# Optimization experiments

Hardware: AMD Instinct MI355X
Metric: run time of the kernel (lower is better)

## Reference

```python
import jax, jax.numpy as jnp
import numpy as np

N, H, W = 128, 128, 128
K = 9          # 3x3 kernel points
DIL = 3        # dilation of the deformable conv


def conv2d(x, w, pad, dil):
    # x: [N,C,H,W], w: [O,I,kh,kw]
    return jax.lax.conv_general_dilated(
        x, w, (1, 1), [(pad, pad), (pad, pad)], rhs_dilation=(dil, dil),
        dimension_numbers=("NCHW", "OIHW", "NCHW"))


def _bilinear_one(img, py, px):
    # img: [C,H,W]; py, px: [K,H,W] sample coords. Zero outside borders (DCNv2 semantics).
    Hh, Ww = img.shape[1], img.shape[2]
    y0f = jnp.floor(py)
    x0f = jnp.floor(px)
    y0 = y0f.astype(jnp.int32)
    x0 = x0f.astype(jnp.int32)
    ly = (py - y0f)[None]   # [1,K,H,W]
    lx = (px - x0f)[None]

    def gather(yi, xi):
        valid = ((yi >= 0) & (yi < Hh) & (xi >= 0) & (xi < Ww)).astype(img.dtype)
        yc = jnp.clip(yi, 0, Hh - 1)
        xc = jnp.clip(xi, 0, Ww - 1)
        return img[:, yc, xc] * valid[None]   # [C,K,H,W]

    v00 = gather(y0, x0)
    v01 = gather(y0, x0 + 1)
    v10 = gather(y0 + 1, x0)
    v11 = gather(y0 + 1, x0 + 1)
    return (v00 * (1 - ly) * (1 - lx) + v01 * (1 - ly) * lx
            + v10 * ly * (1 - lx) + v11 * ly * lx)


def modulated_deform_conv(x, offset, mod, w, b):
    # x: [N,C,H,W]; offset: [N,2K,H,W] with (dy,dx) interleaved per kernel point
    # (standard DCNv2 channel layout); mod: [N,K,H,W]; w: [O,C,3,3]; b: [O]
    Np, C, Hh, Ww = x.shape
    dy = offset[:, 0::2]   # [N,K,H,W]
    dx = offset[:, 1::2]
    base_y = ((jnp.repeat(jnp.arange(3), 3) - 1) * DIL).astype(x.dtype)  # [K]
    base_x = ((jnp.tile(jnp.arange(3), 3) - 1) * DIL).astype(x.dtype)
    gy = jnp.arange(Hh, dtype=x.dtype).reshape(1, 1, Hh, 1)
    gx = jnp.arange(Ww, dtype=x.dtype).reshape(1, 1, 1, Ww)
    py = dy + base_y.reshape(1, K, 1, 1) + gy   # [N,K,H,W]
    px = dx + base_x.reshape(1, K, 1, 1) + gx
    samp = jax.vmap(_bilinear_one)(x, py, px)   # [N,C,K,H,W]
    samp = samp * mod[:, None]                  # sigmoid modulation
    out = jnp.einsum("nckij,ock->noij", samp, w.reshape(w.shape[0], C, K))
    return out + b.reshape(1, -1, 1, 1)


def setup_inputs() -> dict:
    key = jax.random.key(0)
    ks = jax.random.split(key, 12)
    f32 = jnp.float32
    return {
        "mask": jax.random.normal(ks[0], (N, 1, H, W), f32),
        "x": jax.random.normal(ks[1], (N, 8, H, W), f32),
        "w1": jax.random.normal(ks[2], (2, 9, 3, 3), f32) * 0.1,      # conv1x1_1 (3x3)
        "b1": jnp.zeros((2,), f32),
        "w_off": jax.random.normal(ks[3], (27, 2, 3, 3), f32) * 0.05,  # offset/mask conv
        "w_dcn": jax.random.normal(ks[4], (2, 2, 3, 3), f32) * 0.2,    # deform conv weight
        "b_dcn": jnp.zeros((2,), f32),
        "w2": jax.random.normal(ks[5], (2, 2, 1, 1), f32) * 0.5,       # conv1x1_2
        "b2": jnp.zeros((2,), f32),
        "fc1_w": jax.random.normal(ks[6], (2048, 2 * 64 * 64), f32) * 0.01,
        "fc1_b": jnp.zeros((2048,), f32),
        "fc2_w": jax.random.normal(ks[7], (1024, 2048), f32) * 0.02,
        "fc2_b": jnp.zeros((1024,), f32),
        "io_w": jax.random.normal(ks[8], (1, 1024), f32) * 0.01,
        "io_b": jnp.zeros((1,), f32),
    }


def reference(mask, x, w1, b1, w_off, w_dcn, b_dcn, w2, b2,
              fc1_w, fc1_b, fc2_w, fc2_b, io_w, io_b):
    z = jnp.concatenate([x, mask], axis=1)                    # [N,9,H,W]
    h = conv2d(z, w1, 1, 1) + b1.reshape(1, -1, 1, 1)          # [N,2,H,W]
    om = conv2d(h, w_off, 3, 3)                               # [N,27,H,W], bias=False
    ox, oy, mm = jnp.split(om, 3, axis=1)
    offset = jnp.concatenate([ox, oy], axis=1)                # [N,18,H,W]
    mm = jax.nn.sigmoid(mm)                                   # [N,9,H,W]
    h = modulated_deform_conv(h, offset, mm, w_dcn, b_dcn)    # [N,2,H,W]
    h = jax.nn.relu(conv2d(h, w2, 0, 1) + b2.reshape(1, -1, 1, 1))
    Np, C, Hh, Ww = h.shape                                   # adaptive max pool to 64x64
    h = h.reshape(Np, C, 64, Hh // 64, 64, Ww // 64).max(axis=(3, 5))
    h = h.reshape(Np, -1)                                     # [N, 8192]
    h = jax.nn.relu(h @ fc1_w.T + fc1_b)
    h = jax.nn.relu(h @ fc2_w.T + fc2_b)
    return jax.nn.sigmoid(h @ io_w.T + io_b)                  # [N,1]
```

## Files before the change

### kernel.cpp

```cpp
#include <hip/hip_runtime.h>
#include <math.h>

#define NB   128
#define HH   128
#define WW   128
#define HW   (HH*WW)
#define POOLD 64
#define FC1_IN  8192
#define FC1_OUT 2048
#define FC2_OUT 1024

#define H1_OFF    0
#define POOL_OFF  4194304
#define FC1_OFF   5242880
#define FC2_OFF   5505024

__global__ __launch_bounds__(256) void conv1_kernel(
    const float* __restrict__ xin, const float* __restrict__ mask,
    const float* __restrict__ w1, const float* __restrict__ b1,
    float* __restrict__ h1)
{
    __shared__ float sw[164];
    __shared__ float sh[9][10][132];

    int tid = threadIdx.x;
    int n   = blockIdx.y;
    int r0  = blockIdx.x * 8;

    if (tid < 162) sw[tid] = w1[tid];
    if (tid < 2)   sw[162 + tid] = b1[tid];

    for (int i = tid; i < 90; i += 256) {
        int c  = i / 10;
        int ry = i - c * 10;
        sh[c][ry][0]   = 0.f;
        sh[c][ry][129] = 0.f;
    }

    for (int idx = tid; idx < 2880; idx += 256) {
        int c   = idx / 320;
        int rem = idx - c * 320;
        int ry  = rem >> 5;
        int x4  = (rem & 31) << 2;
        int g   = r0 - 1 + ry;
        float4 v = make_float4(0.f, 0.f, 0.f, 0.f);
        if (g >= 0 && g < HH) {
            const float* src = (c < 8) ? (xin + ((size_t)n * 8 + c) * HW)
                                       : (mask + (size_t)n * HW);
            v = *(const float4*)(src + (size_t)g * WW + x4);
        }
        float* d = &sh[c][ry][x4 + 1];
        d[0] = v.x; d[1] = v.y; d[2] = v.z; d[3] = v.w;
    }
    __syncthreads();

    int x  = tid & 127;
    int yb = (tid >> 7) * 4;

    float acc[4][2];
    #pragma unroll
    for (int r = 0; r < 4; ++r) { acc[r][0] = sw[162]; acc[r][1] = sw[163]; }

    for (int c = 0; c < 9; ++c) {
        float v[6][3];
        #pragma unroll
        for (int iy = 0; iy < 6; ++iy)
            #pragma unroll
            for (int kx = 0; kx < 3; ++kx)
                v[iy][kx] = sh[c][yb + iy][x + kx];
        #pragma unroll
        for (int r = 0; r < 4; ++r)
            #pragma unroll
            for (int ky = 0; ky < 3; ++ky)
                #pragma unroll
                for (int kx = 0; kx < 3; ++kx) {
                    float t = v[r + ky][kx];
                    acc[r][0] += t * sw[c * 9 + ky * 3 + kx];
                    acc[r][1] += t * sw[81 + c * 9 + ky * 3 + kx];
                }
    }

    #pragma unroll
    for (int r = 0; r < 4; ++r) {
        size_t base = (size_t)n * (2 * HW) + (size_t)(r0 + yb + r) * WW + x;
        h1[base]      = acc[r][0];
        h1[base + HW] = acc[r][1];
    }
}

#define HALO 8

__device__ __forceinline__ void fetch2(
    const float* __restrict__ sh, const float* __restrict__ h0,
    const float* __restrict__ hb, int row_lo, int row_hi,
    int yi, int xi, float& a, float& b)
{
    a = 0.f; b = 0.f;
    if (yi < 0 || yi >= HH || xi < 0 || xi >= WW) return;
    if (yi >= row_lo && yi < row_hi) {
        const float* p = sh + ((size_t)(yi - row_lo) * WW + xi) * 2;
        a = p[0]; b = p[1];
    } else {
        a = h0[yi * WW + xi];
        b = hb[yi * WW + xi];
    }
}

__global__ __launch_bounds__(256, 4) void fused_dcn_kernel(
    const float* __restrict__ h1,
    const float* __restrict__ w_off,
    const float* __restrict__ w_dcn,
    const float* __restrict__ b_dcn,
    const float* __restrict__ w2,
    const float* __restrict__ b2,
    float* __restrict__ pooled)
{
    __shared__ float sh[32 * WW * 2];
    __shared__ float sw[530];

    int tid = threadIdx.x;
    int n   = blockIdx.y;
    int r0  = blockIdx.x * 16;

    for (int i = tid; i < 530; i += 256) {
        float v;
        if (i < 486)      v = w_off[i];
        else if (i < 522) v = w_dcn[i - 486];
        else if (i < 526) v = w2[i - 522];
        else if (i < 528) v = b_dcn[i - 526];
        else              v = b2[i - 528];
        sw[i] = v;
    }

    int row_lo = r0 - HALO;       if (row_lo < 0)   row_lo = 0;
    int row_hi = r0 + 16 + HALO;  if (row_hi > HH)  row_hi = HH;
    int rows = row_hi - row_lo;

    const float* h0 = h1 + (size_t)n * (2 * HW);
    const float* hb = h0 + HW;

    for (int idx = tid; idx < rows * 32; idx += 256) {
        int ry = idx >> 5;
        int x4 = (idx & 31) << 2;
        const float4 a = *(const float4*)(h0 + (size_t)(row_lo + ry) * WW + x4);
        const float4 b = *(const float4*)(hb + (size_t)(row_lo + ry) * WW + x4);
        float* d = sh + ((size_t)ry * WW + x4) * 2;
        d[0] = a.x; d[1] = b.x; d[2] = a.y; d[3] = b.y;
        d[4] = a.z; d[5] = b.z; d[6] = a.w; d[7] = b.w;
    }
    __syncthreads();

    const float* WOFF = sw;
    const float* WDCN = sw + 486;
    const float* W2   = sw + 522;
    const float* BDCN = sw + 526;
    const float* B2   = sw + 528;

    int pc  = tid & 63;
    int prb = blockIdx.x * 8 + (tid >> 6);

    #pragma unroll 1
    for (int i = 0; i < 2; ++i) {
        int pr = prb + 4 * i;
        float m0 = -1e30f, m1 = -1e30f;

        #pragma unroll 1
        for (int s = 0; s < 4; ++s) {
            int y = pr * 2 + (s >> 1);
            int x = pc * 2 + (s & 1);

            float hvx[9], hvy[9];
            #pragma unroll
            for (int t = 0; t < 9; ++t) {
                int yy = y + (t / 3 - 1) * 3;
                int xx = x + (t % 3 - 1) * 3;
                float a = 0.f, b = 0.f;
                if (yy >= 0 && yy < HH && xx >= 0 && xx < WW) {
                    const float* p = sh + ((size_t)(yy - row_lo) * WW + xx) * 2;
                    a = p[0]; b = p[1];
                }
                hvx[t] = a; hvy[t] = b;
            }

            float acc0 = 0.f, acc1 = 0.f;
            #pragma unroll 1
            for (int k = 0; k < 9; ++k) {
                const float* wy = WOFF + (2 * k) * 18;
                const float* wx = WOFF + (2 * k + 1) * 18;
                const float* wm = WOFF + (18 + k) * 18;
                float dyv = 0.f, dxv = 0.f, mv = 0.f;
                #pragma unroll
                for (int t = 0; t < 9; ++t) {
                    float ha = hvx[t], hcb = hvy[t];
                    dyv += ha * wy[t] + hcb * wy[9 + t];
                    dxv += ha * wx[t] + hcb * wx[9 + t];
                    mv  += ha * wm[t] + hcb * wm[9 + t];
                }
                float mod = 1.f / (1.f + __expf(-mv));

                float py  = (float)(y + (k / 3 - 1) * 3) + dyv;
                float pxx = (float)(x + (k % 3 - 1) * 3) + dxv;
                float y0f = floorf(py), x0f = floorf(pxx);
                int   y0 = (int)y0f,   x0 = (int)x0f;
                float ly = py - y0f,   lx = pxx - x0f;

                float a00, b00, a01, b01, a10, b10, a11, b11;
                fetch2(sh, h0, hb, row_lo, row_hi, y0,     x0,     a00, b00);
                fetch2(sh, h0, hb, row_lo, row_hi, y0,     x0 + 1, a01, b01);
                fetch2(sh, h0, hb, row_lo, row_hi, y0 + 1, x0,     a10, b10);
                fetch2(sh, h0, hb, row_lo, row_hi, y0 + 1, x0 + 1, a11, b11);

                float w00 = (1.f - ly) * (1.f - lx);
                float w01 = (1.f - ly) * lx;
                float w10 = ly * (1.f - lx);
                float w11 = ly * lx;
                float sA = (w00 * a00 + w01 * a01 + w10 * a10 + w11 * a11) * mod;
                float sB = (w00 * b00 + w01 * b01 + w10 * b10 + w11 * b11) * mod;

                acc0 += WDCN[k]      * sA + WDCN[9 + k]  * sB;
                acc1 += WDCN[18 + k] * sA + WDCN[27 + k] * sB;
            }

            float v0 = acc0 + BDCN[0];
            float v1 = acc1 + BDCN[1];
            float u0 = fmaxf(W2[0] * v0 + W2[1] * v1 + B2[0], 0.f);
            float u1 = fmaxf(W2[2] * v0 + W2[3] * v1 + B2[1], 0.f);
            m0 = fmaxf(m0, u0);
            m1 = fmaxf(m1, u1);
        }

        size_t pb = (size_t)n * FC1_IN + (size_t)pr * POOLD + pc;
        pooled[pb]        = m0;
        pooled[pb + 4096] = m1;
    }
}

__global__ void init_bias2_kernel(
    float* __restrict__ o1, const float* __restrict__ bb1,
    float* __restrict__ o2, const float* __restrict__ bb2)
{
    int i = blockIdx.x * blockDim.x + threadIdx.x;
    if (i < NB * FC1_OUT) o1[i] = bb1[i & (FC1_OUT - 1)];
    if (i < NB * FC2_OUT) o2[i] = bb2[i & (FC2_OUT - 1)];
}

typedef __bf16 bf16x8 __attribute__((ext_vector_type(8)));
typedef float  f32x4  __attribute__((ext_vector_type(4)));

#define LDT 40

__device__ __forceinline__ unsigned short f2bf(float f) {
    unsigned int u = __float_as_uint(f);
    return (unsigned short)((u + 0x7fffu + ((u >> 16) & 1u)) >> 16);
}

__global__ __launch_bounds__(256) void gemm_bf16_splitk(
    const float* __restrict__ A, const float* __restrict__ B,
    float* __restrict__ C, int K, int Nc, int kchunk, int relu_a)
{
    __shared__ __align__(16) unsigned short As[128 * LDT];
    __shared__ __align__(16) unsigned short Bs[64 * LDT];

    int tid = threadIdx.x;
    int jt  = blockIdx.x;
    int k0  = blockIdx.y * kchunk;
    int iters = kchunk >> 5;

    int t8  = tid >> 3;
    int c16 = (tid & 7) << 2;

    const float* Ag = A + (size_t)t8 * K + k0 + c16;
    const float* Bg = B + (size_t)(jt * 64 + t8) * K + k0 + c16;

    float4 pa[4]; float4 pb[2];
    #pragma unroll
    for (int p = 0; p < 4; ++p) pa[p] = *(const float4*)(Ag + (size_t)(p * 32) * K);
    #pragma unroll
    for (int p = 0; p < 2; ++p) pb[p] = *(const float4*)(Bg + (size_t)(p * 32) * K);

    int lane = tid & 63;
    int w    = tid >> 6;
    int quad = lane >> 4;
    int r    = lane & 15;

    f32x4 acc[2][4];
    #pragma unroll
    for (int mt = 0; mt < 2; ++mt)
        #pragma unroll
        for (int nt = 0; nt < 4; ++nt)
            acc[mt][nt] = (f32x4){0.f, 0.f, 0.f, 0.f};

    for (int it = 0; it < iters; ++it) {
        #pragma unroll
        for (int p = 0; p < 4; ++p) {
            float4 v = pa[p];
            if (relu_a) {
                v.x = fmaxf(v.x, 0.f); v.y = fmaxf(v.y, 0.f);
                v.z = fmaxf(v.z, 0.f); v.w = fmaxf(v.w, 0.f);
            }
            ushort4 s = make_ushort4(f2bf(v.x), f2bf(v.y), f2bf(v.z), f2bf(v.w));
            *(ushort4*)&As[(t8 + p * 32) * LDT + c16] = s;
        }
        #pragma unroll
        for (int p = 0; p < 2; ++p) {
            float4 v = pb[p];
            ushort4 s = make_ushort4(f2bf(v.x), f2bf(v.y), f2bf(v.z), f2bf(v.w));
            *(ushort4*)&Bs[(t8 + p * 32) * LDT + c16] = s;
        }
        __syncthreads();

        if (it + 1 < iters) {
            Ag += 32; Bg += 32;
            #pragma unroll
            for (int p = 0; p < 4; ++p) pa[p] = *(const float4*)(Ag + (size_t)(p * 32) * K);
            #pragma unroll
            for (int p = 0; p < 2; ++p) pb[p] = *(const float4*)(Bg + (size_t)(p * 32) * K);
        }

        bf16x8 af[2];
        #pragma unroll
        for (int mt = 0; mt < 2; ++mt)
            af[mt] = *(const bf16x8*)&As[(w * 32 + mt * 16 + r) * LDT + quad * 8];
        bf16x8 bfr[4];
        #pragma unroll
        for (int nt = 0; nt < 4; ++nt)
            bfr[nt] = *(const bf16x8*)&Bs[(nt * 16 + r) * LDT + quad * 8];

        #pragma unroll
        for (int mt = 0; mt < 2; ++mt)
            #pragma unroll
            for (int nt = 0; nt < 4; ++nt)
                acc[mt][nt] = __builtin_amdgcn_mfma_f32_16x16x32_bf16(
                    af[mt], bfr[nt], acc[mt][nt], 0, 0, 0);

        __syncthreads();
    }

    #pragma unroll
    for (int mt = 0; mt < 2; ++mt) {
        int mrow = w * 32 + mt * 16 + quad * 4;
        #pragma unroll
        for (int nt = 0; nt < 4; ++nt) {
            int col = jt * 64 + nt * 16 + r;
            #pragma unroll
            for (int i = 0; i < 4; ++i)
                atomicAdd(C + (size_t)(mrow + i) * Nc + col, acc[mt][nt][i]);
        }
    }
}

__global__ __launch_bounds__(256) void io_kernel(
    const float* __restrict__ fc2o, const float* __restrict__ io_w,
    const float* __restrict__ io_b, float* __restrict__ out)
{
    int n = blockIdx.x;
    int tid = threadIdx.x;
    float s = 0.f;
    #pragma unroll
    for (int k = tid; k < FC2_OUT; k += 256)
        s += fmaxf(fc2o[(size_t)n * FC2_OUT + k], 0.f) * io_w[k];
    #pragma unroll
    for (int off = 32; off > 0; off >>= 1)
        s += __shfl_down(s, off, 64);
    __shared__ float red[4];
    if ((tid & 63) == 0) red[tid >> 6] = s;
    __syncthreads();
    if (tid == 0) {
        float t = red[0] + red[1] + red[2] + red[3] + io_b[0];
        out[n] = 1.f / (1.f + expf(-t));
    }
}

extern "C" void kernel_launch(void* const* d_in, const int* in_sizes, int n_in,
                              void* d_out, int out_size, void* d_ws, size_t ws_size,
                              hipStream_t stream)
{
    const float* mask  = (const float*)d_in[0];
    const float* x     = (const float*)d_in[1];
    const float* w1    = (const float*)d_in[2];
    const float* b1    = (const float*)d_in[3];
    const float* w_off = (const float*)d_in[4];
    const float* w_dcn = (const float*)d_in[5];
    const float* b_dcn = (const float*)d_in[6];
    const float* w2    = (const float*)d_in[7];
    const float* b2    = (const float*)d_in[8];
    const float* fc1_w = (const float*)d_in[9];
    const float* fc1_b = (const float*)d_in[10];
    const float* fc2_w = (const float*)d_in[11];
    const float* fc2_b = (const float*)d_in[12];
    const float* io_w  = (const float*)d_in[13];
    const float* io_b  = (const float*)d_in[14];

    float* ws      = (float*)d_ws;
    float* h1      = ws + H1_OFF;
    float* pooled  = ws + POOL_OFF;
    float* fc1_out = ws + FC1_OFF;
    float* fc2_out = ws + FC2_OFF;
    float* out     = (float*)d_out;

    conv1_kernel<<<dim3(16, NB), 256, 0, stream>>>(x, mask, w1, b1, h1);

    fused_dcn_kernel<<<dim3(8, NB), 256, 0, stream>>>(
        h1, w_off, w_dcn, b_dcn, w2, b2, pooled);

    init_bias2_kernel<<<(NB * FC1_OUT + 255) / 256, 256, 0, stream>>>(
        fc1_out, fc1_b, fc2_out, fc2_b);

    gemm_bf16_splitk<<<dim3(FC1_OUT / 64, 16), 256, 0, stream>>>(
        pooled, fc1_w, fc1_out, FC1_IN, FC1_OUT, FC1_IN / 16, 0);

    gemm_bf16_splitk<<<dim3(FC2_OUT / 64, 16), 256, 0, stream>>>(
        fc1_out, fc2_w, fc2_out, FC1_OUT, FC2_OUT, FC1_OUT / 16, 1);

    io_kernel<<<NB, 256, 0, stream>>>(fc2_out, io_w, io_b, out);
}
```

Before: 334.2 us.

## Restructure DCN kernel to share offset weights across four pooled pixels

The loop order inside the fused DCN kernel is swapped so each kernel point k handles all four pixels of a 2x2 pool window together, which reuses each offset-conv weight load four times. Weights are repacked in shared memory as interleaved float2/float4. The shared tile gets zero padding columns and rows so the hot path can do unconditional float2 loads and a single bounds check per bilinear sample. The cost is higher register pressure, reflected in dropping launch_bounds occupancy from 4 to 3, plus a larger shared tile.

```diff
diff --git a/kernel.cpp b/kernel.cpp
--- a/kernel.cpp
+++ b/kernel.cpp
@@ -88,25 +88,15 @@
     }
 }
 
-#define HALO 8
-
-__device__ __forceinline__ void fetch2(
-    const float* __restrict__ sh, const float* __restrict__ h0,
-    const float* __restrict__ hb, int row_lo, int row_hi,
-    int yi, int xi, float& a, float& b)
-{
-    a = 0.f; b = 0.f;
-    if (yi < 0 || yi >= HH || xi < 0 || xi >= WW) return;
-    if (yi >= row_lo && yi < row_hi) {
-        const float* p = sh + ((size_t)(yi - row_lo) * WW + xi) * 2;
-        a = p[0]; b = p[1];
-    } else {
-        a = h0[yi * WW + xi];
-        b = hb[yi * WW + xi];
-    }
-}
-
-__global__ __launch_bounds__(256, 4) void fused_dcn_kernel(
+#define ROWB 32
+#define COLB 136
+
+__device__ __forceinline__ float gatg(const float* __restrict__ hc, int yi, int xi)
+{
+    return (yi >= 0 && yi < HH && xi >= 0 && xi < WW) ? hc[yi * WW + xi] : 0.f;
+}
+
+__global__ __launch_bounds__(256, 3) void fused_dcn_kernel(
     const float* __restrict__ h1,
     const float* __restrict__ w_off,
     const float* __restrict__ w_dcn,
@@ -115,46 +105,61 @@
     const float* __restrict__ b2,
     float* __restrict__ pooled)
 {
-    __shared__ float sh[32 * WW * 2];
-    __shared__ float sw[530];
+    __shared__ float sh[ROWB * COLB * 2];
+    __shared__ float swr[532];
 
     int tid = threadIdx.x;
     int n   = blockIdx.y;
     int r0  = blockIdx.x * 16;
-
-    for (int i = tid; i < 530; i += 256) {
-        float v;
-        if (i < 486)      v = w_off[i];
-        else if (i < 522) v = w_dcn[i - 486];
-        else if (i < 526) v = w2[i - 522];
-        else if (i < 528) v = b_dcn[i - 526];
-        else              v = b2[i - 528];
-        sw[i] = v;
-    }
-
-    int row_lo = r0 - HALO;       if (row_lo < 0)   row_lo = 0;
-    int row_hi = r0 + 16 + HALO;  if (row_hi > HH)  row_hi = HH;
-    int rows = row_hi - row_lo;
+    int row_base = r0 - 8;
+
+    for (int i = tid; i < 532; i += 256) {
+        float v = 0.f;
+        if (i < 486) {
+            int k = i / 54, r = i - k * 54;
+            int o = r / 18, q = r - o * 18;
+            int t = q >> 1, c = q & 1;
+            int srow = (o == 0) ? 2 * k : (o == 1) ? (2 * k + 1) : (18 + k);
+            v = w_off[srow * 18 + c * 9 + t];
+        } else if (i >= 488 && i < 524) {
+            int j = i - 488;
+            int k = j >> 2, oc = (j >> 1) & 1, c = j & 1;
+            v = w_dcn[oc * 18 + c * 9 + k];
+        } else if (i >= 524 && i < 528) v = w2[i - 524];
+        else if (i >= 528 && i < 530)   v = b_dcn[i - 528];
+        else if (i >= 530)              v = b2[i - 530];
+        swr[i] = v;
+    }
 
     const float* h0 = h1 + (size_t)n * (2 * HW);
     const float* hb = h0 + HW;
 
-    for (int idx = tid; idx < rows * 32; idx += 256) {
+    for (int idx = tid; idx < 1024; idx += 256) {
         int ry = idx >> 5;
         int x4 = (idx & 31) << 2;
-        const float4 a = *(const float4*)(h0 + (size_t)(row_lo + ry) * WW + x4);
-        const float4 b = *(const float4*)(hb + (size_t)(row_lo + ry) * WW + x4);
-        float* d = sh + ((size_t)ry * WW + x4) * 2;
+        int gy = row_base + ry;
+        float4 a = make_float4(0.f, 0.f, 0.f, 0.f);
+        float4 b = make_float4(0.f, 0.f, 0.f, 0.f);
+        if (gy >= 0 && gy < HH) {
+            a = *(const float4*)(h0 + (size_t)gy * WW + x4);
+            b = *(const float4*)(hb + (size_t)gy * WW + x4);
+        }
+        float* d = sh + ((size_t)ry * COLB + x4 + 4) * 2;
         d[0] = a.x; d[1] = b.x; d[2] = a.y; d[3] = b.y;
         d[4] = a.z; d[5] = b.z; d[6] = a.w; d[7] = b.w;
     }
+    {
+        int ry   = tid >> 3;
+        int pcix = tid & 7;
+        int rx   = (pcix < 4) ? pcix : (128 + pcix);
+        float* d = sh + ((size_t)ry * COLB + rx) * 2;
+        d[0] = 0.f; d[1] = 0.f;
+    }
     __syncthreads();
 
-    const float* WOFF = sw;
-    const float* WDCN = sw + 486;
-    const float* W2   = sw + 522;
-    const float* BDCN = sw + 526;
-    const float* B2   = sw + 528;
+    const float* W2   = swr + 524;
+    const float* BDCN = swr + 528;
+    const float* B2   = swr + 530;
 
     int pc  = tid & 63;
     int prb = blockIdx.x * 8 + (tid >> 6);
@@ -162,53 +167,73 @@
     #pragma unroll 1
     for (int i = 0; i < 2; ++i) {
         int pr = prb + 4 * i;
-        float m0 = -1e30f, m1 = -1e30f;
+
+        float2 hv[4][9];
+        #pragma unroll
+        for (int sp = 0; sp < 4; ++sp) {
+            int y  = pr * 2 + (sp >> 1);
+            int x  = pc * 2 + (sp & 1);
+            const float* base = sh + (((size_t)(y - row_base - 3)) * COLB + (x + 1)) * 2;
+            #pragma unroll
+            for (int ty = 0; ty < 3; ++ty)
+                #pragma unroll
+                for (int tx = 0; tx < 3; ++tx)
+                    hv[sp][ty * 3 + tx] =
+                        *(const float2*)(base + ((size_t)ty * 3 * COLB + tx * 3) * 2);
+        }
+
+        float acc0[4] = {0.f, 0.f, 0.f, 0.f};
+        float acc1[4] = {0.f, 0.f, 0.f, 0.f};
 
         #pragma unroll 1
-        for (int s = 0; s < 4; ++s) {
-            int y = pr * 2 + (s >> 1);
-            int x = pc * 2 + (s & 1);
-
-            float hvx[9], hvy[9];
+        for (int k = 0; k < 9; ++k) {
+            const float* wb = swr + k * 54;
+            float dyv[4] = {0.f, 0.f, 0.f, 0.f};
+            float dxv[4] = {0.f, 0.f, 0.f, 0.f};
+            float mv[4]  = {0.f, 0.f, 0.f, 0.f};
             #pragma unroll
             for (int t = 0; t < 9; ++t) {
-                int yy = y + (t / 3 - 1) * 3;
-                int xx = x + (t % 3 - 1) * 3;
-                float a = 0.f, b = 0.f;
-                if (yy >= 0 && yy < HH && xx >= 0 && xx < WW) {
-                    const float* p = sh + ((size_t)(yy - row_lo) * WW + xx) * 2;
-                    a = p[0]; b = p[1];
+                float2 wy = *(const float2*)(wb + t * 2);
+                float2 wx = *(const float2*)(wb + 18 + t * 2);
+                float2 wm = *(const float2*)(wb + 36 + t * 2);
+                #pragma unroll
+                for (int sp = 0; sp < 4; ++sp) {
+                    float2 h = hv[sp][t];
+                    dyv[sp] += h.x * wy.x + h.y * wy.y;
+                    dxv[sp] += h.x * wx.x + h.y * wx.y;
+                    mv[sp]  += h.x * wm.x + h.y * wm.y;
                 }
-                hvx[t] = a; hvy[t] = b;
             }
 
-            float acc0 = 0.f, acc1 = 0.f;
-            #pragma unroll 1
-            for (int k = 0; k < 9; ++k) {
-                const float* wy = WOFF + (2 * k) * 18;
-                const float* wx = WOFF + (2 * k + 1) * 18;
-                const float* wm = WOFF + (18 + k) * 18;
-                float dyv = 0.f, dxv = 0.f, mv = 0.f;
-                #pragma unroll
-                for (int t = 0; t < 9; ++t) {
-                    float ha = hvx[t], hcb = hvy[t];
-                    dyv += ha * wy[t] + hcb * wy[9 + t];
-                    dxv += ha * wx[t] + hcb * wx[9 + t];
-                    mv  += ha * wm[t] + hcb * wm[9 + t];
+            float4 wd = *(const float4*)(swr + 488 + k * 4);
+            int kdy = (k / 3 - 1) * 3;
+            int kdx = (k % 3 - 1) * 3;
+
+            #pragma unroll
+            for (int sp = 0; sp < 4; ++sp) {
+                int y = pr * 2 + (sp >> 1);
+                int x = pc * 2 + (sp & 1);
+                float mod = 1.f / (1.f + __expf(-mv[sp]));
+                float py  = (float)(y + kdy) + dyv[sp];
+                float px  = (float)(x + kdx) + dxv[sp];
+                float y0f = floorf(py), x0f = floorf(px);
+                int   y0 = (int)y0f,   x0 = (int)x0f;
+                float ly = py - y0f,   lx = px - x0f;
+
+                int ry0 = y0 - row_base;
+                int rx0 = x0 + 4;
+                float a00, b00, a01, b01, a10, b10, a11, b11;
+                if ((unsigned)ry0 < 31u && (unsigned)rx0 < 135u) {
+                    const float* p = sh + ((size_t)ry0 * COLB + rx0) * 2;
+                    a00 = p[0]; b00 = p[1]; a01 = p[2]; b01 = p[3];
+                    const float* q = p + COLB * 2;
+                    a10 = q[0]; b10 = q[1]; a11 = q[2]; b11 = q[3];
+                } else {
+                    a00 = gatg(h0, y0, x0);     b00 = gatg(hb, y0, x0);
+                    a01 = gatg(h0, y0, x0 + 1); b01 = gatg(hb, y0, x0 + 1);
+                    a10 = gatg(h0, y0 + 1, x0); b10 = gatg(hb, y0 + 1, x0);
+                    a11 = gatg(h0, y0 + 1, x0 + 1); b11 = gatg(hb, y0 + 1, x0 + 1);
                 }
-                float mod = 1.f / (1.f + __expf(-mv));
-
-                float py  = (float)(y + (k / 3 - 1) * 3) + dyv;
-                float pxx = (float)(x + (k % 3 - 1) * 3) + dxv;
-                float y0f = floorf(py), x0f = floorf(pxx);
-                int   y0 = (int)y0f,   x0 = (int)x0f;
-                float ly = py - y0f,   lx = pxx - x0f;
-
-                float a00, b00, a01, b01, a10, b10, a11, b11;
-                fetch2(sh, h0, hb, row_lo, row_hi, y0,     x0,     a00, b00);
-                fetch2(sh, h0, hb, row_lo, row_hi, y0,     x0 + 1, a01, b01);
-                fetch2(sh, h0, hb, row_lo, row_hi, y0 + 1, x0,     a10, b10);
-                fetch2(sh, h0, hb, row_lo, row_hi, y0 + 1, x0 + 1, a11, b11);
 
                 float w00 = (1.f - ly) * (1.f - lx);
                 float w01 = (1.f - ly) * lx;
@@ -216,13 +241,16 @@
                 float w11 = ly * lx;
                 float sA = (w00 * a00 + w01 * a01 + w10 * a10 + w11 * a11) * mod;
                 float sB = (w00 * b00 + w01 * b01 + w10 * b10 + w11 * b11) * mod;
-
-                acc0 += WDCN[k]      * sA + WDCN[9 + k]  * sB;
-                acc1 += WDCN[18 + k] * sA + WDCN[27 + k] * sB;
+                acc0[sp] += wd.x * sA + wd.y * sB;
+                acc1[sp] += wd.z * sA + wd.w * sB;
             }
-
-            float v0 = acc0 + BDCN[0];
-            float v1 = acc1 + BDCN[1];
+        }
+
+        float m0 = -1e30f, m1 = -1e30f;
+        #pragma unroll
+        for (int sp = 0; sp < 4; ++sp) {
+            float v0 = acc0[sp] + BDCN[0];
+            float v1 = acc1[sp] + BDCN[1];
             float u0 = fmaxf(W2[0] * v0 + W2[1] * v1 + B2[0], 0.f);
             float u1 = fmaxf(W2[2] * v0 + W2[3] * v1 + B2[1], 0.f);
             m0 = fmaxf(m0, u0);
```

New measurement: 361.1 us. 1.08x slower.
